# Kernel optimization log

Measured on AMD Instinct MI355X. Metric: run time of the kernel, lower is better.

The kernel has to match this reference:

```python
import jax, jax.numpy as jnp
import numpy as np
from jax.experimental.jet import jet

ORDER = 3  # Taylor order from init_kwargs
D, C, H = 4096, 4096, 8192


def setup_inputs() -> dict:
    key = jax.random.key(0)
    k = jax.random.split(key, 6)
    sc1 = 1.0 / np.sqrt(D + C)
    sc2 = 1.0 / np.sqrt(H)
    return {
        "h": jax.random.normal(k[0], (D,), jnp.float32),
        "r": jnp.zeros((), jnp.float32),  # ignored residual slot of h_r tuple
        "t": jax.random.uniform(k[1], (), jnp.float32),
        "c": jax.random.normal(k[2], (C,), jnp.float32),
        "W1": jax.random.normal(k[3], (D + C, H), jnp.float32) * sc1,
        "b1": jnp.zeros((H,), jnp.float32),
        "W2": jax.random.normal(k[4], (H, D), jnp.float32) * sc2,
        "b2": jnp.zeros((D,), jnp.float32),
    }


def reference(h, r, t, c, W1, b1, W2, b2):
    # dynamics f(h, t, c): 2-layer tanh MLP on concat(h, c)
    def f(_h, _t, _c):
        x = jnp.concatenate((_h, _c))
        return jnp.tanh(x @ W1 + b1) @ W2 + b2

    h_shape = h.shape

    def g(h_t):
        # expand flattened state+time through dynamics
        _h, _t = jnp.reshape(h_t[:-1], h_shape), h_t[-1]
        dh = jnp.ravel(f(_h, _t, c))
        return jnp.concatenate((dh, jnp.array([1.0], dtype=dh.dtype)))

    h_t = jnp.concatenate((jnp.ravel(h), jnp.reshape(t, (1,))))
    # recursive Taylor-mode jet expansion
    (y0, [*yns]) = jet(g, (h_t,), ((jnp.ones_like(h_t),),))
    for _ in range(ORDER - 1):
        (y0, [*yns]) = jet(g, (h_t,), ((y0, *yns),))
    dydt = jnp.reshape(y0[:-1], h_shape)
    drdt = jnp.reshape(yns[-2][:-1], h_shape)
    return (dydt, jnp.mean(drdt ** 2))
```

## Files before the change

kernel.cpp:

```cpp
#include <hip/hip_runtime.h>

#define DD 4096
#define HH 8192

enum Stage { S_X0 = 0, S_TANH, S_BIASOUT, S_PMUL, S_COPY, S_S2 };

typedef float vfloat4 __attribute__((ext_vector_type(4)));

template <bool NT, int KS, int NTOT>
__device__ inline void stream_cols(const float* __restrict__ Wp,
                                   const float* __restrict__ xs,
                                   float* __restrict__ op) {
    float ax = 0.f, ay = 0.f, az = 0.f, aw = 0.f;
#pragma unroll 8
    for (int k = 0; k < KS; ++k) {
        const float xv = xs[k];
        const float* row = Wp + (size_t)k * NTOT;
        vfloat4 w;
        if constexpr (NT)
            w = __builtin_nontemporal_load(reinterpret_cast<const vfloat4*>(row));
        else
            w = *reinterpret_cast<const vfloat4*>(row);
        ax = fmaf(xv, w.x, ax);
        ay = fmaf(xv, w.y, ay);
        az = fmaf(xv, w.z, az);
        aw = fmaf(xv, w.w, aw);
    }
    *reinterpret_cast<float4*>(op) = make_float4(ax, ay, az, aw);
}

template <int STAGE, int KS, int SPREV, int KPREV, int NTOT, int BX, int NTMODE>
__global__ __launch_bounds__(256) void gemv_phase(
    const float* __restrict__ W, const float* __restrict__ Pprev,
    float* __restrict__ Pout,
    const float* __restrict__ h, const float* __restrict__ c,
    const float* __restrict__ b1, const float* __restrict__ b2,
    float* __restrict__ s0g, float* __restrict__ t0g, float* __restrict__ a1g,
    float* __restrict__ outv)
{
    constexpr int GROUPS = 256 / KS;
    __shared__ float xs[KS];
    __shared__ float part[GROUPS * KS];
    const int tid = threadIdx.x;
    const int bx = blockIdx.x;
    const int by = blockIdx.y;
    const int k0 = by * KS;

    if constexpr (STAGE == S_X0) {
        if (tid < KS) {
            int k = k0 + tid;
            xs[tid] = (k < DD) ? h[k] : c[k - DD];
        }
    } else {
        const int g = tid / KS, j = tid % KS;
        float acc = 0.f;
        for (int s = g; s < SPREV; s += GROUPS)
            acc += Pprev[(size_t)s * KPREV + k0 + j];
        part[g * KS + j] = acc;
        __syncthreads();
        if (tid < KS) {
            const int k = k0 + tid;
            float tot = 0.f;
#pragma unroll
            for (int g2 = 0; g2 < GROUPS; ++g2) tot += part[g2 * KS + tid];
            float xv;
            if constexpr (STAGE == S_TANH) {
                float s = tanhf(tot + b1[k]);
                xv = s;
                if (bx == 0) { s0g[k] = s; t0g[k] = 1.f - s * s; }
            } else if constexpr (STAGE == S_BIASOUT) {
                xv = tot + b2[k];
                if (bx == 0) outv[k] = xv;
            } else if constexpr (STAGE == S_PMUL) {
                xv = t0g[k] * tot;
                if (bx == 0) a1g[k] = tot;
            } else if constexpr (STAGE == S_COPY) {
                xv = tot;
            } else {
                float a1v = a1g[k];
                xv = t0g[k] * (tot - s0g[k] * a1v * a1v);
            }
            xs[tid] = xv;
        }
    }
    __syncthreads();

    const int ncol = bx * 1024 + tid * 4;
    const float* Wp = W + (size_t)k0 * NTOT + ncol;
    float* op = Pout + (size_t)by * NTOT + ncol;

    if constexpr (NTMODE == 0) {
        stream_cols<false, KS, NTOT>(Wp, xs, op);
    } else if constexpr (NTMODE == 1) {
        stream_cols<true, KS, NTOT>(Wp, xs, op);
    } else {
        if (k0 >= DD) stream_cols<true, KS, NTOT>(Wp, xs, op);
        else          stream_cols<false, KS, NTOT>(Wp, xs, op);
    }
}

template <int SPREV>
__global__ __launch_bounds__(256) void reduce_sq_partial(const float* __restrict__ P6,
                                                         float* __restrict__ partial) {
    const int n = blockIdx.x * 256 + threadIdx.x;
    float acc = 0.f;
#pragma unroll 8
    for (int s = 0; s < SPREV; ++s) acc += P6[(size_t)s * DD + n];
    float sq = acc * acc;
    for (int off = 32; off; off >>= 1) sq += __shfl_down(sq, off);
    __shared__ float ls[4];
    const int wid = threadIdx.x >> 6;
    if ((threadIdx.x & 63) == 0) ls[wid] = sq;
    __syncthreads();
    if (threadIdx.x == 0) partial[blockIdx.x] = ls[0] + ls[1] + ls[2] + ls[3];
}

__global__ __launch_bounds__(64) void finalize_meansq(const float* __restrict__ partial,
                                                      float* __restrict__ dout) {
    float v = (threadIdx.x < 16) ? partial[threadIdx.x] : 0.f;
    for (int off = 8; off; off >>= 1) v += __shfl_down(v, off);
    if (threadIdx.x == 0) dout[DD] = v / (float)DD;
}

extern "C" void kernel_launch(void* const* d_in, const int* in_sizes, int n_in,
                              void* d_out, int out_size, void* d_ws, size_t ws_size,
                              hipStream_t stream) {
    const float* h  = (const float*)d_in[0];
    const float* c  = (const float*)d_in[3];
    const float* W1 = (const float*)d_in[4];
    const float* b1 = (const float*)d_in[5];
    const float* W2 = (const float*)d_in[6];
    const float* b2 = (const float*)d_in[7];
    float* out = (float*)d_out;
    float* ws = (float*)d_ws;

    float* P1 = ws;
    float* P2 = P1 + 1048576;
    float* P3 = P2 + 1048576;
    float* P4 = P3 + 1048576;
    float* P5 = P4 + 1048576;
    float* P6 = P5 + 1048576;
    float* s0 = P6 + 1048576;
    float* t0 = s0 + 8192;
    float* a1 = t0 + 8192;
    float* psum = a1 + 8192;

    gemv_phase<S_X0, 64, 1, 1, HH, 8, 2><<<dim3(8, 128), 256, 0, stream>>>(
        W1, nullptr, P1, h, c, b1, b2, s0, t0, a1, out);
    gemv_phase<S_TANH, 32, 128, HH, DD, 4, 0><<<dim3(4, 256), 256, 0, stream>>>(
        W2, P1, P2, h, c, b1, b2, s0, t0, a1, out);
    gemv_phase<S_BIASOUT, 32, 256, DD, HH, 8, 0><<<dim3(8, 128), 256, 0, stream>>>(
        W1, P2, P3, h, c, b1, b2, s0, t0, a1, out);
    gemv_phase<S_PMUL, 32, 128, HH, DD, 4, 0><<<dim3(4, 256), 256, 0, stream>>>(
        W2, P3, P4, h, c, b1, b2, s0, t0, a1, out);
    gemv_phase<S_COPY, 32, 256, DD, HH, 8, 1><<<dim3(8, 128), 256, 0, stream>>>(
        W1, P4, P5, h, c, b1, b2, s0, t0, a1, out);
    gemv_phase<S_S2, 32, 128, HH, DD, 4, 1><<<dim3(4, 256), 256, 0, stream>>>(
        W2, P5, P6, h, c, b1, b2, s0, t0, a1, out);
    reduce_sq_partial<256><<<16, 256, 0, stream>>>(P6, psum);
    finalize_meansq<<<1, 64, 0, stream>>>(psum, out);
}
```

Baseline: 212.0 us.

## Convert W1 h-rows to bf16 in first pass and stream bf16 in later W1 GEMVs

The first W1 GEMV now also writes a bf16 copy of the h-part rows of W1 (first 4096 rows) into workspace. The two later W1 GEMVs (bias-out and copy stages) read this bf16 copy instead of the fp32 weights, which halves their weight traffic, and they use 8 columns per thread with a K-split of 16. This trades extra write traffic in the first kernel and reduced weight precision for lower memory bandwidth in the later W1 passes.

```diff
diff --git a/kernel.cpp b/kernel.cpp
--- a/kernel.cpp
+++ b/kernel.cpp
@@ -7,10 +7,17 @@
 
 typedef float vfloat4 __attribute__((ext_vector_type(4)));
 
-template <bool NT, int KS, int NTOT>
-__device__ inline void stream_cols(const float* __restrict__ Wp,
-                                   const float* __restrict__ xs,
-                                   float* __restrict__ op) {
+__device__ inline unsigned short f2bf(float f) {
+    unsigned int u = __float_as_uint(f);
+    u += 0x7FFFu + ((u >> 16) & 1u);
+    return (unsigned short)(u >> 16);
+}
+
+template <bool NT, bool CONV, int KS, int NTOT>
+__device__ inline void stream_f32(const float* __restrict__ Wp,
+                                  const float* __restrict__ xs,
+                                  float* __restrict__ op,
+                                  unsigned short* __restrict__ Wbp) {
     float ax = 0.f, ay = 0.f, az = 0.f, aw = 0.f;
 #pragma unroll 8
     for (int k = 0; k < KS; ++k) {
@@ -25,27 +32,25 @@
         ay = fmaf(xv, w.y, ay);
         az = fmaf(xv, w.z, az);
         aw = fmaf(xv, w.w, aw);
+        if constexpr (CONV) {
+            ushort4 o;
+            o.x = f2bf(w.x); o.y = f2bf(w.y); o.z = f2bf(w.z); o.w = f2bf(w.w);
+            *reinterpret_cast<ushort4*>(Wbp + (size_t)k * NTOT) = o;
+        }
     }
     *reinterpret_cast<float4*>(op) = make_float4(ax, ay, az, aw);
 }
 
-template <int STAGE, int KS, int SPREV, int KPREV, int NTOT, int BX, int NTMODE>
-__global__ __launch_bounds__(256) void gemv_phase(
-    const float* __restrict__ W, const float* __restrict__ Pprev,
-    float* __restrict__ Pout,
-    const float* __restrict__ h, const float* __restrict__ c,
-    const float* __restrict__ b1, const float* __restrict__ b2,
-    float* __restrict__ s0g, float* __restrict__ t0g, float* __restrict__ a1g,
-    float* __restrict__ outv)
+template <int STAGE, int KS, int SPREV, int KPREV>
+__device__ inline void prologue(const float* __restrict__ Pprev,
+                                const float* __restrict__ h, const float* __restrict__ c,
+                                const float* __restrict__ b1, const float* __restrict__ b2,
+                                float* __restrict__ s0g, float* __restrict__ t0g,
+                                float* __restrict__ a1g, float* __restrict__ outv,
+                                float* xs, float* part, int k0, int bx)
 {
     constexpr int GROUPS = 256 / KS;
-    __shared__ float xs[KS];
-    __shared__ float part[GROUPS * KS];
     const int tid = threadIdx.x;
-    const int bx = blockIdx.x;
-    const int by = blockIdx.y;
-    const int k0 = by * KS;
-
     if constexpr (STAGE == S_X0) {
         if (tid < KS) {
             int k = k0 + tid;
@@ -84,19 +89,75 @@
         }
     }
     __syncthreads();
-
-    const int ncol = bx * 1024 + tid * 4;
+}
+
+template <int STAGE, int KS, int SPREV, int KPREV, int NTOT, int NTMODE, bool CONV>
+__global__ __launch_bounds__(256) void gemv_f32(
+    const float* __restrict__ W, const float* __restrict__ Pprev,
+    float* __restrict__ Pout, unsigned short* __restrict__ Wb,
+    const float* __restrict__ h, const float* __restrict__ c,
+    const float* __restrict__ b1, const float* __restrict__ b2,
+    float* __restrict__ s0g, float* __restrict__ t0g, float* __restrict__ a1g,
+    float* __restrict__ outv)
+{
+    __shared__ float xs[KS];
+    __shared__ float part[256];
+    const int bx = blockIdx.x, by = blockIdx.y;
+    const int k0 = by * KS;
+    prologue<STAGE, KS, SPREV, KPREV>(Pprev, h, c, b1, b2, s0g, t0g, a1g, outv,
+                                      xs, part, k0, bx);
+
+    const int ncol = bx * 1024 + threadIdx.x * 4;
     const float* Wp = W + (size_t)k0 * NTOT + ncol;
     float* op = Pout + (size_t)by * NTOT + ncol;
+    unsigned short* Wbp = CONV ? (Wb + (size_t)k0 * NTOT + ncol) : nullptr;
 
     if constexpr (NTMODE == 0) {
-        stream_cols<false, KS, NTOT>(Wp, xs, op);
+        stream_f32<false, false, KS, NTOT>(Wp, xs, op, nullptr);
     } else if constexpr (NTMODE == 1) {
-        stream_cols<true, KS, NTOT>(Wp, xs, op);
+        stream_f32<true, false, KS, NTOT>(Wp, xs, op, nullptr);
     } else {
-        if (k0 >= DD) stream_cols<true, KS, NTOT>(Wp, xs, op);
-        else          stream_cols<false, KS, NTOT>(Wp, xs, op);
-    }
+        if (k0 >= DD) stream_f32<true, false, KS, NTOT>(Wp, xs, op, nullptr);
+        else          stream_f32<false, CONV, KS, NTOT>(Wp, xs, op, Wbp);
+    }
+}
+
+template <int STAGE, int KS, int SPREV, int KPREV, int NTOT>
+__global__ __launch_bounds__(256) void gemv_b16(
+    const unsigned short* __restrict__ Wb, const float* __restrict__ Pprev,
+    float* __restrict__ Pout,
+    const float* __restrict__ h, const float* __restrict__ c,
+    const float* __restrict__ b1, const float* __restrict__ b2,
+    float* __restrict__ s0g, float* __restrict__ t0g, float* __restrict__ a1g,
+    float* __restrict__ outv)
+{
+    __shared__ float xs[KS];
+    __shared__ float part[256];
+    const int bx = blockIdx.x, by = blockIdx.y;
+    const int k0 = by * KS;
+    prologue<STAGE, KS, SPREV, KPREV>(Pprev, h, c, b1, b2, s0g, t0g, a1g, outv,
+                                      xs, part, k0, bx);
+
+    const int ncol = bx * 2048 + threadIdx.x * 8;
+    const unsigned short* Wp = Wb + (size_t)k0 * NTOT + ncol;
+    float a0 = 0.f, a1 = 0.f, a2 = 0.f, a3 = 0.f;
+    float a4 = 0.f, a5 = 0.f, a6 = 0.f, a7 = 0.f;
+#pragma unroll 8
+    for (int k = 0; k < KS; ++k) {
+        const float xv = xs[k];
+        const uint4 w = *reinterpret_cast<const uint4*>(Wp + (size_t)k * NTOT);
+        a0 = fmaf(xv, __uint_as_float(w.x << 16), a0);
+        a1 = fmaf(xv, __uint_as_float(w.x & 0xFFFF0000u), a1);
+        a2 = fmaf(xv, __uint_as_float(w.y << 16), a2);
+        a3 = fmaf(xv, __uint_as_float(w.y & 0xFFFF0000u), a3);
+        a4 = fmaf(xv, __uint_as_float(w.z << 16), a4);
+        a5 = fmaf(xv, __uint_as_float(w.z & 0xFFFF0000u), a5);
+        a6 = fmaf(xv, __uint_as_float(w.w << 16), a6);
+        a7 = fmaf(xv, __uint_as_float(w.w & 0xFFFF0000u), a7);
+    }
+    float* op = Pout + (size_t)by * NTOT + ncol;
+    *reinterpret_cast<float4*>(op)     = make_float4(a0, a1, a2, a3);
+    *reinterpret_cast<float4*>(op + 4) = make_float4(a4, a5, a6, a7);
 }
 
 template <int SPREV>
@@ -137,26 +198,27 @@
     float* P1 = ws;
     float* P2 = P1 + 1048576;
     float* P3 = P2 + 1048576;
-    float* P4 = P3 + 1048576;
+    float* P4 = P3 + 2097152;
     float* P5 = P4 + 1048576;
-    float* P6 = P5 + 1048576;
+    float* P6 = P5 + 2097152;
     float* s0 = P6 + 1048576;
     float* t0 = s0 + 8192;
     float* a1 = t0 + 8192;
     float* psum = a1 + 8192;
-
-    gemv_phase<S_X0, 64, 1, 1, HH, 8, 2><<<dim3(8, 128), 256, 0, stream>>>(
-        W1, nullptr, P1, h, c, b1, b2, s0, t0, a1, out);
-    gemv_phase<S_TANH, 32, 128, HH, DD, 4, 0><<<dim3(4, 256), 256, 0, stream>>>(
-        W2, P1, P2, h, c, b1, b2, s0, t0, a1, out);
-    gemv_phase<S_BIASOUT, 32, 256, DD, HH, 8, 0><<<dim3(8, 128), 256, 0, stream>>>(
-        W1, P2, P3, h, c, b1, b2, s0, t0, a1, out);
-    gemv_phase<S_PMUL, 32, 128, HH, DD, 4, 0><<<dim3(4, 256), 256, 0, stream>>>(
-        W2, P3, P4, h, c, b1, b2, s0, t0, a1, out);
-    gemv_phase<S_COPY, 32, 256, DD, HH, 8, 1><<<dim3(8, 128), 256, 0, stream>>>(
-        W1, P4, P5, h, c, b1, b2, s0, t0, a1, out);
-    gemv_phase<S_S2, 32, 128, HH, DD, 4, 1><<<dim3(4, 256), 256, 0, stream>>>(
-        W2, P5, P6, h, c, b1, b2, s0, t0, a1, out);
+    unsigned short* W1b = (unsigned short*)(psum + 64);
+
+    gemv_f32<S_X0, 64, 1, 1, HH, 2, true><<<dim3(8, 128), 256, 0, stream>>>(
+        W1, nullptr, P1, W1b, h, c, b1, b2, s0, t0, a1, out);
+    gemv_f32<S_TANH, 32, 128, HH, DD, 0, false><<<dim3(4, 256), 256, 0, stream>>>(
+        W2, P1, P2, nullptr, h, c, b1, b2, s0, t0, a1, out);
+    gemv_b16<S_BIASOUT, 16, 256, DD, HH><<<dim3(4, 256), 256, 0, stream>>>(
+        W1b, P2, P3, h, c, b1, b2, s0, t0, a1, out);
+    gemv_f32<S_PMUL, 32, 256, HH, DD, 0, false><<<dim3(4, 256), 256, 0, stream>>>(
+        W2, P3, P4, nullptr, h, c, b1, b2, s0, t0, a1, out);
+    gemv_b16<S_COPY, 16, 256, DD, HH><<<dim3(4, 256), 256, 0, stream>>>(
+        W1b, P4, P5, h, c, b1, b2, s0, t0, a1, out);
+    gemv_f32<S_S2, 32, 256, HH, DD, 1, false><<<dim3(4, 256), 256, 0, stream>>>(
+        W2, P5, P6, nullptr, h, c, b1, b2, s0, t0, a1, out);
     reduce_sq_partial<256><<<16, 256, 0, stream>>>(P6, psum);
     finalize_meansq<<<1, 64, 0, stream>>>(psum, out);
 }
```

New measurement: 202.8 us. 1.05x faster.
